# Performance work log

Measured on AMD Instinct MI355X. Metric: run time of the kernel, lower is better.

The kernel has to match this reference:

```python
import jax, jax.numpy as jnp
import numpy as np

ALPHA, GAMMA, EPS = 0.25, 2.0, 1e-8
COST_CLASS, COST_BBOX, COST_GIOU = 2.0, 5.0, 2.0


def box_cxcywh_to_xyxy(b):
    cx, cy, w, h = jnp.split(b, 4, axis=-1)
    return jnp.concatenate([cx - 0.5 * w, cy - 0.5 * h, cx + 0.5 * w, cy + 0.5 * h], axis=-1)


def setup_inputs() -> dict:
    key = jax.random.key(0)
    k1, k2, k3, k4 = jax.random.split(key, 4)
    bs, Q, C, T = 16, 900, 80, 1600
    return {
        "pred_logits": jax.random.normal(k1, (bs, Q, C), jnp.float32),
        "pred_boxes": jax.random.uniform(k2, (bs, Q, 4), jnp.float32),
        "tgt_labels": jax.random.randint(k3, (T,), 0, C),
        "tgt_boxes": jax.random.uniform(k4, (T, 4), jnp.float32),
        "g_size": 3,
    }


def reference(pred_logits, pred_boxes, tgt_labels, tgt_boxes, g_size):
    bs, Q, _ = pred_logits.shape
    # focal classification cost (use_focal=True path)
    p = jax.nn.sigmoid(pred_logits.reshape(bs * Q, -1))  # [N, C]
    neg = (1.0 - ALPHA) * p ** GAMMA * (-jnp.log(1.0 - p + EPS))
    pos = ALPHA * (1.0 - p) ** GAMMA * (-jnp.log(p + EPS))
    cost_class = (pos - neg)[:, tgt_labels]  # [N, T]
    # L1 box cost (cdist p=1)
    out_bbox = pred_boxes.reshape(bs * Q, 4)
    cost_bbox = jnp.abs(out_bbox[:, None, :] - tgt_bbox_b(tgt_boxes)).sum(-1)  # [N, T]
    # GIoU cost
    b1 = box_cxcywh_to_xyxy(out_bbox)  # [N, 4]
    b2 = box_cxcywh_to_xyxy(tgt_boxes)  # [T, 4]
    area1 = (b1[:, 2] - b1[:, 0]) * (b1[:, 3] - b1[:, 1])
    area2 = (b2[:, 2] - b2[:, 0]) * (b2[:, 3] - b2[:, 1])
    lt = jnp.maximum(b1[:, None, :2], b2[None, :, :2])
    rb = jnp.minimum(b1[:, None, 2:], b2[None, :, 2:])
    wh = jnp.clip(rb - lt, 0.0)
    inter = wh[..., 0] * wh[..., 1]
    union = area1[:, None] + area2[None, :] - inter
    iou = inter / union
    elt = jnp.minimum(b1[:, None, :2], b2[None, :, :2])
    erb = jnp.maximum(b1[:, None, 2:], b2[None, :, 2:])
    ewh = jnp.clip(erb - elt, 0.0)
    earea = ewh[..., 0] * ewh[..., 1]
    giou = iou - (earea - union) / earea
    # weighted total cost, then group reduction (note: original names it Cmin but takes max over the group dim)
    Cmat = COST_BBOX * cost_bbox + COST_CLASS * cost_class + COST_GIOU * (-giou)
    Cmin = Cmat.reshape(bs, Q // g_size, g_size, -1).max(axis=2)  # [bs, Q//g, T]
    return Cmin


def tgt_bbox_b(tgt_boxes):
    return tgt_boxes[None, :, :]
```

## Files before the change

kernel.cpp:

```cpp
#include <hip/hip_runtime.h>

#define ALPHA 0.25f
#define EPS   1e-8f

constexpr int BS = 16;
constexpr int QN = 900;
constexpr int CN = 80;
constexpr int GS = 3;
constexpr int QG_PER_BLOCK = 4;

__global__ __launch_bounds__(256) void focal_table_kernel(
    const float* __restrict__ logits, float* __restrict__ cc, int total)
{
    int i = blockIdx.x * 256 + threadIdx.x;
    if (i >= total) return;
    float x = logits[i];
    float p = 1.0f / (1.0f + expf(-x));
    float omp = 1.0f - p;
    float pos = ALPHA * omp * omp * (-logf(p + EPS));
    float neg = (1.0f - ALPHA) * p * p * (-logf(omp + EPS));
    cc[i] = pos - neg;
}

__global__ __launch_bounds__(256) void cost_kernel(
    const float* __restrict__ pred_boxes,
    const float* __restrict__ tgt_boxes,
    const int*   __restrict__ tgt_labels,
    const float* __restrict__ cc,
    float*       __restrict__ out,
    int T)
{
    __shared__ float4 s_raw[QG_PER_BLOCK * GS];
    __shared__ float4 s_xy [QG_PER_BLOCK * GS];
    __shared__ float  s_ar [QG_PER_BLOCK * GS];
    __shared__ float  s_cc [QG_PER_BLOCK * GS * CN];

    const int tid = threadIdx.x;
    const int qg0 = blockIdx.y * QG_PER_BLOCK;
    const int b   = blockIdx.z;
    const int n0  = b * QN + qg0 * GS;

    if (tid < QG_PER_BLOCK * GS) {
        const float4 r = ((const float4*)pred_boxes)[n0 + tid];
        s_raw[tid] = r;
        float x0 = r.x - 0.5f * r.z, y0 = r.y - 0.5f * r.w;
        float x1 = r.x + 0.5f * r.z, y1 = r.y + 0.5f * r.w;
        s_xy[tid] = make_float4(x0, y0, x1, y1);
        s_ar[tid] = (x1 - x0) * (y1 - y0);
    }
    for (int k = tid; k < QG_PER_BLOCK * GS * CN; k += 256)
        s_cc[k] = cc[n0 * CN + k];
    __syncthreads();

    const int t = blockIdx.x * 256 + tid;
    if (t >= T) return;

    const float4 tr = ((const float4*)tgt_boxes)[t];
    const float tx0 = tr.x - 0.5f * tr.z, ty0 = tr.y - 0.5f * tr.w;
    const float tx1 = tr.x + 0.5f * tr.z, ty1 = tr.y + 0.5f * tr.w;
    const float ta  = (tx1 - tx0) * (ty1 - ty0);
    const int lab   = tgt_labels[t];

    const int qgTotal = QN / GS;
    #pragma unroll
    for (int j = 0; j < QG_PER_BLOCK; ++j) {
        float m = -3.402823466e+38f;
        #pragma unroll
        for (int g = 0; g < GS; ++g) {
            const int idx = j * GS + g;
            const float4 pr = s_raw[idx];
            const float4 px = s_xy[idx];
            const float  pa = s_ar[idx];
            const float  ccv = s_cc[idx * CN + lab];

            float l1 = fabsf(pr.x - tr.x) + fabsf(pr.y - tr.y)
                     + fabsf(pr.z - tr.z) + fabsf(pr.w - tr.w);

            float ix0 = fmaxf(px.x, tx0), iy0 = fmaxf(px.y, ty0);
            float ix1 = fminf(px.z, tx1), iy1 = fminf(px.w, ty1);
            float iw = fmaxf(ix1 - ix0, 0.0f), ih = fmaxf(iy1 - iy0, 0.0f);
            float inter = iw * ih;
            float uni   = pa + ta - inter;

            float ex0 = fminf(px.x, tx0), ey0 = fminf(px.y, ty0);
            float ex1 = fmaxf(px.z, tx1), ey1 = fmaxf(px.w, ty1);
            float ew = fmaxf(ex1 - ex0, 0.0f), eh = fmaxf(ey1 - ey0, 0.0f);
            float earea = ew * eh;

            float giou = __fdividef(inter, uni) + __fdividef(uni, earea) - 1.0f;

            float cost = 5.0f * l1 + 2.0f * ccv - 2.0f * giou;
            m = fmaxf(m, cost);
        }
        const int qg = qg0 + j;
        out[((size_t)(b * qgTotal + qg)) * T + t] = m;
    }
}

extern "C" void kernel_launch(void* const* d_in, const int* in_sizes, int n_in,
                              void* d_out, int out_size, void* d_ws, size_t ws_size,
                              hipStream_t stream) {
    const float* pred_logits = (const float*)d_in[0];
    const float* pred_boxes  = (const float*)d_in[1];
    const int*   tgt_labels  = (const int*)d_in[2];
    const float* tgt_boxes   = (const float*)d_in[3];

    const int T = in_sizes[2];
    const int totalNC = in_sizes[0];

    float* cc = (float*)d_ws;
    float* out = (float*)d_out;

    focal_table_kernel<<<(totalNC + 255) / 256, 256, 0, stream>>>(
        pred_logits, cc, totalNC);

    dim3 grid((T + 255) / 256, (QN / GS) / QG_PER_BLOCK, BS);
    cost_kernel<<<grid, 256, 0, stream>>>(
        pred_boxes, tgt_boxes, tgt_labels, cc, out, T);
}
```

Measured before the change: 107.9 us.

## Fuse focal table into cost kernel and loop targets within each block

```diff
diff --git a/kernel.cpp b/kernel.cpp
--- a/kernel.cpp
+++ b/kernel.cpp
@@ -8,92 +8,84 @@
 constexpr int CN = 80;
 constexpr int GS = 3;
 constexpr int QG_PER_BLOCK = 4;
+constexpr int ROWS = QG_PER_BLOCK * GS;
+constexpr int NT_THREADS = 256;
 
-__global__ __launch_bounds__(256) void focal_table_kernel(
-    const float* __restrict__ logits, float* __restrict__ cc, int total)
-{
-    int i = blockIdx.x * 256 + threadIdx.x;
-    if (i >= total) return;
-    float x = logits[i];
-    float p = 1.0f / (1.0f + expf(-x));
-    float omp = 1.0f - p;
-    float pos = ALPHA * omp * omp * (-logf(p + EPS));
-    float neg = (1.0f - ALPHA) * p * p * (-logf(omp + EPS));
-    cc[i] = pos - neg;
-}
-
-__global__ __launch_bounds__(256) void cost_kernel(
+__global__ __launch_bounds__(NT_THREADS) void fused_cost_kernel(
+    const float* __restrict__ pred_logits,
     const float* __restrict__ pred_boxes,
+    const int*   __restrict__ tgt_labels,
     const float* __restrict__ tgt_boxes,
-    const int*   __restrict__ tgt_labels,
-    const float* __restrict__ cc,
     float*       __restrict__ out,
     int T)
 {
-    __shared__ float4 s_raw[QG_PER_BLOCK * GS];
-    __shared__ float4 s_xy [QG_PER_BLOCK * GS];
-    __shared__ float  s_ar [QG_PER_BLOCK * GS];
-    __shared__ float  s_cc [QG_PER_BLOCK * GS * CN];
+    __shared__ float4 s_raw[ROWS];
+    __shared__ float4 s_xy [ROWS];
+    __shared__ float  s_cc [ROWS * CN];
 
     const int tid = threadIdx.x;
-    const int qg0 = blockIdx.y * QG_PER_BLOCK;
-    const int b   = blockIdx.z;
+    const int qg0 = blockIdx.x * QG_PER_BLOCK;
+    const int b   = blockIdx.y;
     const int n0  = b * QN + qg0 * GS;
 
-    if (tid < QG_PER_BLOCK * GS) {
+    if (tid < ROWS) {
         const float4 r = ((const float4*)pred_boxes)[n0 + tid];
         s_raw[tid] = r;
-        float x0 = r.x - 0.5f * r.z, y0 = r.y - 0.5f * r.w;
-        float x1 = r.x + 0.5f * r.z, y1 = r.y + 0.5f * r.w;
-        s_xy[tid] = make_float4(x0, y0, x1, y1);
-        s_ar[tid] = (x1 - x0) * (y1 - y0);
+        s_xy[tid]  = make_float4(r.x - 0.5f * r.z, r.y - 0.5f * r.w,
+                                 r.x + 0.5f * r.z, r.y + 0.5f * r.w);
     }
-    for (int k = tid; k < QG_PER_BLOCK * GS * CN; k += 256)
-        s_cc[k] = cc[n0 * CN + k];
+    const float* lg0 = pred_logits + (size_t)n0 * CN;
+    #pragma unroll
+    for (int k = tid; k < ROWS * CN; k += NT_THREADS) {
+        float x = lg0[k];
+        float p = __fdividef(1.0f, 1.0f + __expf(-x));
+        float omp = 1.0f - p;
+        float pos = ALPHA * omp * omp * (-__logf(p + EPS));
+        float neg = (1.0f - ALPHA) * p * p * (-__logf(omp + EPS));
+        s_cc[k] = pos - neg;
+    }
     __syncthreads();
 
-    const int t = blockIdx.x * 256 + tid;
-    if (t >= T) return;
+    const int qgTotal = QN / GS;
+    const size_t outBase = (size_t)(b * qgTotal + qg0) * T;
 
-    const float4 tr = ((const float4*)tgt_boxes)[t];
-    const float tx0 = tr.x - 0.5f * tr.z, ty0 = tr.y - 0.5f * tr.w;
-    const float tx1 = tr.x + 0.5f * tr.z, ty1 = tr.y + 0.5f * tr.w;
-    const float ta  = (tx1 - tx0) * (ty1 - ty0);
-    const int lab   = tgt_labels[t];
+    for (int t = tid; t < T; t += NT_THREADS) {
+        const float4 tr = ((const float4*)tgt_boxes)[t];
+        const float tx0 = tr.x - 0.5f * tr.z, ty0 = tr.y - 0.5f * tr.w;
+        const float tx1 = tr.x + 0.5f * tr.z, ty1 = tr.y + 0.5f * tr.w;
+        const float ta  = tr.z * tr.w;
+        const int lab   = tgt_labels[t];
 
-    const int qgTotal = QN / GS;
-    #pragma unroll
-    for (int j = 0; j < QG_PER_BLOCK; ++j) {
-        float m = -3.402823466e+38f;
         #pragma unroll
-        for (int g = 0; g < GS; ++g) {
-            const int idx = j * GS + g;
-            const float4 pr = s_raw[idx];
-            const float4 px = s_xy[idx];
-            const float  pa = s_ar[idx];
-            const float  ccv = s_cc[idx * CN + lab];
+        for (int j = 0; j < QG_PER_BLOCK; ++j) {
+            float m = -3.402823466e+38f;
+            #pragma unroll
+            for (int g = 0; g < GS; ++g) {
+                const int idx = j * GS + g;
+                const float4 pr = s_raw[idx];
+                const float4 px = s_xy[idx];
+                const float  ccv = s_cc[idx * CN + lab];
+                const float  pa = pr.z * pr.w;
 
-            float l1 = fabsf(pr.x - tr.x) + fabsf(pr.y - tr.y)
-                     + fabsf(pr.z - tr.z) + fabsf(pr.w - tr.w);
+                float l1 = fabsf(pr.x - tr.x) + fabsf(pr.y - tr.y)
+                         + fabsf(pr.z - tr.z) + fabsf(pr.w - tr.w);
 
-            float ix0 = fmaxf(px.x, tx0), iy0 = fmaxf(px.y, ty0);
-            float ix1 = fminf(px.z, tx1), iy1 = fminf(px.w, ty1);
-            float iw = fmaxf(ix1 - ix0, 0.0f), ih = fmaxf(iy1 - iy0, 0.0f);
-            float inter = iw * ih;
-            float uni   = pa + ta - inter;
+                float iw = fminf(px.z, tx1) - fmaxf(px.x, tx0);
+                float ih = fminf(px.w, ty1) - fmaxf(px.y, ty0);
+                float inter = fmaxf(iw, 0.0f) * fmaxf(ih, 0.0f);
+                float uni   = pa + ta - inter;
 
-            float ex0 = fminf(px.x, tx0), ey0 = fminf(px.y, ty0);
-            float ex1 = fmaxf(px.z, tx1), ey1 = fmaxf(px.w, ty1);
-            float ew = fmaxf(ex1 - ex0, 0.0f), eh = fmaxf(ey1 - ey0, 0.0f);
-            float earea = ew * eh;
+                float ew = fmaxf(px.z, tx1) - fminf(px.x, tx0);
+                float eh = fmaxf(px.w, ty1) - fminf(px.y, ty0);
+                float earea = ew * eh;
 
-            float giou = __fdividef(inter, uni) + __fdividef(uni, earea) - 1.0f;
+                float giou = __fdividef(inter, uni) + __fdividef(uni, earea) - 1.0f;
 
-            float cost = 5.0f * l1 + 2.0f * ccv - 2.0f * giou;
-            m = fmaxf(m, cost);
+                float cost = 5.0f * l1 + 2.0f * ccv - 2.0f * giou;
+                m = fmaxf(m, cost);
+            }
+            out[outBase + (size_t)j * T + t] = m;
         }
-        const int qg = qg0 + j;
-        out[((size_t)(b * qgTotal + qg)) * T + t] = m;
     }
 }
 
@@ -106,15 +98,9 @@
     const float* tgt_boxes   = (const float*)d_in[3];
 
     const int T = in_sizes[2];
-    const int totalNC = in_sizes[0];
-
-    float* cc = (float*)d_ws;
     float* out = (float*)d_out;
 
-    focal_table_kernel<<<(totalNC + 255) / 256, 256, 0, stream>>>(
-        pred_logits, cc, totalNC);
-
-    dim3 grid((T + 255) / 256, (QN / GS) / QG_PER_BLOCK, BS);
-    cost_kernel<<<grid, 256, 0, stream>>>(
-        pred_boxes, tgt_boxes, tgt_labels, cc, out, T);
+    dim3 grid((QN / GS) / QG_PER_BLOCK, BS);
+    fused_cost_kernel<<<grid, NT_THREADS, 0, stream>>>(
+        pred_logits, pred_boxes, tgt_labels, tgt_boxes, out, T);
 }
```

Measured after the change: 107.7 us. Within noise of the previous version (-0.2%).
